# Optimization experiments

Measured on AMD Instinct MI355X. Metric: run time of the kernel, lower is better.

Reference implementation:

```python
import jax, jax.numpy as jnp
import numpy as np


def _segsum(v, idx, n):
    return jax.ops.segment_sum(v, idx, num_segments=n)


def _rdl(z, n_dst, Wna, We, Wi, es, ed, is_, id_):
    """Relationship_Decoupled_layer: node softmax attn + per-edge attn.
    e-channel (mode etype): softmax over 2 logits; i-channel: sigmoid(1 logit)."""
    zd = z[:n_dst]
    node_alpha = jax.nn.softmax(zd @ Wna, axis=1)                      # [nd,2]
    e_e = jax.nn.softmax(jnp.concatenate([z[es], zd[ed]], axis=-1) @ We, axis=1)  # [Ee,2]
    e_i = jax.nn.sigmoid(jnp.concatenate([z[is_], zd[id_]], axis=-1) @ Wi)        # [Ei,1]
    return node_alpha, e_e, e_i


def _one_agg(z, n_dst, W, b, na, e_e, es, ed):
    """One_Neighbor_Aggregation: mean over nbrs of e[:,0]*Linear(z_src), relu, + alpha0*z_dst.
    Linear is applied on src nodes once (linearity) instead of per-edge."""
    zd = na[:, 0:1] * z[:n_dst]
    wz = z @ W + b                                                     # [n_src,D]
    s = _segsum(e_e[:, 0:1] * wz[es], ed, n_dst)                       # [nd,D]
    deg = _segsum(jnp.ones((es.shape[0], 1), z.dtype), ed, n_dst)
    f = jax.nn.relu(s / jnp.maximum(deg, 1.0))
    return f + zd


def _nia(z, n_dst, na, e_e, es, ed, e_i, is_, id_):
    """Neighbor_Interaction_Aggregation: e_h (mode etype, attn col 1) and i_h
    (other etype, sigmoid attn), cross term via polarization identity, + alpha1*z_dst."""
    zd = na[:, 1:2] * z[:n_dst]
    e_h = _segsum(e_e[:, 1:2] * z[es], ed, n_dst)
    i_h = _segsum(e_i * z[is_], id_, n_dst)
    inter = jax.nn.relu(0.5 * (jnp.square(e_h + i_h) - jnp.square(e_h) - jnp.square(i_h)))
    return inter + zd


def setup_inputs() -> dict:
    key = jax.random.key(0)
    ks = jax.random.split(key, 32)
    F, D, O = 256, 128, 64
    n_src0, n_dst0, E0 = 100000, 25000, 500000
    n_src1, n_dst1, E1 = 25000, 5000, 100000

    def ri(k, n, hi):
        return jax.random.randint(k, (n,), 0, hi, dtype=jnp.int32)

    inp = {
        'feat': jax.random.normal(ks[0], (n_src0, F), jnp.float32),
        'src0_cor': ri(ks[1], E0, n_src0), 'dst0_cor': ri(ks[2], E0, n_dst0),
        'src0_sim': ri(ks[3], E0, n_src0), 'dst0_sim': ri(ks[4], E0, n_dst0),
        'src1_cor': ri(ks[5], E1, n_src1), 'dst1_cor': ri(ks[6], E1, n_dst1),
        'src1_sim': ri(ks[7], E1, n_src1), 'dst1_sim': ri(ks[8], E1, n_dst1),
        'n_dst0': n_dst0, 'n_dst1': n_dst1,
    }
    s = 0.05  # keep attention logits / activations in a sane range
    inp['Win'] = jax.random.normal(ks[9], (2, F, D)) * s
    inp['b_in'] = jnp.zeros((2, D), jnp.float32)
    inp['na1'] = jax.random.normal(ks[10], (2, D, 2)) * s
    inp['ea1'] = jax.random.normal(ks[11], (2, 2 * D, 2)) * s
    inp['ia1'] = jax.random.normal(ks[12], (2, 2 * D, 1)) * s
    inp['W1'] = jax.random.normal(ks[13], (2, D, D)) * s
    inp['b1'] = jnp.zeros((2, D), jnp.float32)
    inp['na2'] = jax.random.normal(ks[14], (2, D, 2)) * s
    inp['ea2'] = jax.random.normal(ks[15], (2, 2 * D, 2)) * s
    inp['ia2'] = jax.random.normal(ks[16], (2, 2 * D, 1)) * s
    inp['W2'] = jax.random.normal(ks[17], (2, D, D)) * s
    inp['b2'] = jnp.zeros((2, D), jnp.float32)
    inp['Wout'] = jax.random.normal(ks[18], (2, D, O)) * s
    inp['bout'] = jnp.zeros((2, O), jnp.float32)
    return inp


def reference(feat, src0_cor, dst0_cor, src0_sim, dst0_sim,
              src1_cor, dst1_cor, src1_sim, dst1_sim, n_dst0, n_dst1,
              Win, b_in, na1, ea1, ia1, W1, b1, na2, ea2, ia2, W2, b2, Wout, bout):
    # mode index 0 = 'cor', 1 = 'sim'; e-channel = mode etype, i-channel = other etype
    blk0 = {0: (src0_cor, dst0_cor, src0_sim, dst0_sim),
            1: (src0_sim, dst0_sim, src0_cor, dst0_cor)}
    blk1 = {0: (src1_cor, dst1_cor, src1_sim, dst1_sim),
            1: (src1_sim, dst1_sim, src1_cor, dst1_cor)}
    outs = []
    for m in range(2):
        es0, ed0, is0, id0 = blk0[m]
        es1, ed1, is1, id1 = blk1[m]
        z = feat @ Win[m] + b_in[m]                                    # fc_input (eval: dropout = identity)
        # layer 1 on block0
        na, ee, ei = _rdl(z, n_dst0, na1[m], ea1[m], ia1[m], es0, ed0, is0, id0)
        one = _one_agg(z, n_dst0, W1[m], b1[m], na, ee, es0, ed0)
        nia = _nia(z, n_dst0, na, ee, es0, ed0, ei, is0, id0)
        z = 0.5 * (one + nia)                                          # [n_dst0, D]
        # layer 2 on block1
        na, ee, ei = _rdl(z, n_dst1, na2[m], ea2[m], ia2[m], es1, ed1, is1, id1)
        one = _one_agg(z, n_dst1, W2[m], b2[m], na, ee, es1, ed1)
        nia = _nia(z, n_dst1, na, ee, es1, ed1, ei, is1, id1)
        z = 0.5 * (one + nia)                                          # [n_dst1, D]
        outs.append(z @ Wout[m] + bout[m])
    return jnp.stack(outs)                                             # [2, n_dst1, O] (cor, sim)
```

## Files before the change

### kernel.cpp

```cpp
#include <hip/hip_runtime.h>
#include <hip/hip_bf16.h>
#include <math.h>

#define F_DIM 256
#define D_DIM 128
#define O_DIM 64
#define NS0   100000
#define ND0   25000
#define E0_N  500000
#define NS1   25000
#define ND1   5000
#define E1_N  100000

#define NBE0  1954
#define NBE1  391

typedef __attribute__((ext_vector_type(8))) short s8v;
typedef __attribute__((ext_vector_type(4))) float f4v;

struct CPtr4 { const int *p0, *p1, *p2, *p3; };
struct MPtr4 { int *p0, *p1, *p2, *p3; };

__device__ __forceinline__ float2 unpack2(uint u) {
    union { uint i; float f; } a, b;
    a.i = (u & 0xffffu) << 16; b.i = u & 0xffff0000u;
    return make_float2(a.f, b.f);
}
__device__ __forceinline__ ushort f2bf(float f) {
    __hip_bfloat16 h = __float2bfloat16(f);
    return *(ushort*)&h;
}

__global__ void cvt_bf16(const float* __restrict__ in, ushort* __restrict__ out, int n)
{
    int i = (blockIdx.x * 256 + threadIdx.x) * 4;
    if (i >= n) return;
    float4 v = *(const float4*)(in + i);
    ushort4 o;
    o.x = f2bf(v.x); o.y = f2bf(v.y); o.z = f2bf(v.z); o.w = f2bf(v.w);
    *(ushort4*)(out + i) = o;
}

__global__ void prep_weights(
    const float* __restrict__ Win, const float* __restrict__ W1,
    const float* __restrict__ W2,  const float* __restrict__ Wout,
    ushort* __restrict__ Wtin, ushort* __restrict__ Wt1,
    ushort* __restrict__ Wt2,  ushort* __restrict__ Wtout)
{
    int i = blockIdx.x * 256 + threadIdx.x;
    if (i < 65536) {
        int m = i >> 15, r = i & 32767, k = r >> 7, n = r & 127;
        Wtin[m * 32768 + n * 256 + k] = f2bf(Win[m * 32768 + k * 128 + n]);
    } else if (i < 98304) {
        int i2 = i - 65536;
        int m = i2 >> 14, r = i2 & 16383, k = r >> 7, n = r & 127;
        Wt1[m * 16384 + n * 128 + k] = f2bf(W1[m * 16384 + k * 128 + n]);
    } else if (i < 131072) {
        int i2 = i - 98304;
        int m = i2 >> 14, r = i2 & 16383, k = r >> 7, n = r & 127;
        Wt2[m * 16384 + n * 128 + k] = f2bf(W2[m * 16384 + k * 128 + n]);
    } else if (i < 147456) {
        int i2 = i - 131072;
        int m = i2 >> 13, r = i2 & 8191, k = r >> 6, n = r & 63;
        Wtout[m * 8192 + n * 128 + k] = f2bf(Wout[m * 8192 + k * 64 + n]);
    }
}

template<int NW, int KD, int EPI>
__global__ __launch_bounds__(256) void mfma_gemm(
    const ushort* __restrict__ Ab, size_t astr,
    const ushort* __restrict__ Btb, size_t btstr,
    const float* __restrict__ biasb, size_t bstr,
    const float* __restrict__ cvecb, size_t cvstr,
    const float* __restrict__ partialb, size_t pstr,
    void* __restrict__ Coutb, size_t coutstr, int M)
{
    const int m = blockIdx.y;
    const ushort* A  = Ab + m * astr;
    const ushort* Bt = Btb + m * btstr;
    const float* bias = biasb + m * bstr;
    const float* cvec = (EPI == 2) ? cvecb + m * cvstr : nullptr;
    const float* partial = (EPI == 2) ? partialb + m * pstr : nullptr;
    char* Cout = (char*)Coutb + m * coutstr * (EPI == 1 ? 4 : 2);

    constexpr int PA = 40;
    constexpr int WAVES_M = (NW == 128) ? 2 : 4;
    constexpr int WM = 128 / WAVES_M;
    constexpr int TM = WM / 16;
    constexpr int TN = 4;
    __shared__ ushort As[128 * PA];
    __shared__ ushort Bs[NW * PA];

    const int tid  = threadIdx.x;
    const int row0 = blockIdx.x * 128;
    const int wave = tid >> 6, lane = tid & 63;
    const int l15 = lane & 15, l4 = lane >> 4;
    int wm0, wn0;
    if (NW == 128) { wm0 = (wave >> 1) * 64; wn0 = (wave & 1) * 64; }
    else           { wm0 = wave * WM;        wn0 = 0; }

    f4v acc[TM][TN];
    #pragma unroll
    for (int i = 0; i < TM; ++i)
        #pragma unroll
        for (int j = 0; j < TN; ++j)
            acc[i][j] = (f4v)(0.0f);

    for (int kc = 0; kc < KD; kc += 32) {
        __syncthreads();
        #pragma unroll
        for (int it = 0; it < 2; ++it) {
            int f = tid + it * 256;
            int r = f >> 2, g = (f & 3) * 8;
            int gr = row0 + r;
            float4 v = make_float4(0.f, 0.f, 0.f, 0.f);
            if (gr < M) v = *(const float4*)(A + (size_t)gr * KD + kc + g);
            *(float4*)(&As[r * PA + g]) = v;
        }
        #pragma unroll
        for (int it = 0; it < NW * 32 / (256 * 8); ++it) {
            int f = tid + it * 256;
            int r = f >> 2, g = (f & 3) * 8;
            *(float4*)(&Bs[r * PA + g]) = *(const float4*)(Bt + (size_t)r * KD + kc + g);
        }
        __syncthreads();

        s8v af[TM], bfr[TN];
        #pragma unroll
        for (int i = 0; i < TM; ++i)
            af[i] = *(const s8v*)(&As[(wm0 + i * 16 + l15) * PA + l4 * 8]);
        #pragma unroll
        for (int j = 0; j < TN; ++j)
            bfr[j] = *(const s8v*)(&Bs[(wn0 + j * 16 + l15) * PA + l4 * 8]);
        #pragma unroll
        for (int i = 0; i < TM; ++i)
            #pragma unroll
            for (int j = 0; j < TN; ++j)
                acc[i][j] = __builtin_amdgcn_mfma_f32_16x16x32_bf16(
                    af[i], bfr[j], acc[i][j], 0, 0, 0);
    }

    #pragma unroll
    for (int i = 0; i < TM; ++i) {
        #pragma unroll
        for (int ii = 0; ii < 4; ++ii) {
            int row = row0 + wm0 + i * 16 + l4 * 4 + ii;
            if (row < M) {
                #pragma unroll
                for (int j = 0; j < TN; ++j) {
                    int col = wn0 + j * 16 + l15;
                    float a = acc[i][j][ii];
                    if (EPI == 0) {
                        ((ushort*)Cout)[(size_t)row * NW + col] = f2bf(a + bias[col]);
                    } else if (EPI == 1) {
                        ((float*)Cout)[(size_t)row * NW + col] = a + bias[col];
                    } else {
                        float val = a + cvec[row] * bias[col];
                        float o = partial[(size_t)row * NW + col] + 0.5f * fmaxf(val, 0.f);
                        ((ushort*)Cout)[(size_t)row * NW + col] = f2bf(o);
                    }
                }
            }
        }
    }
}

__global__ void histo4(CPtr4 ed, MPtr4 cnt)
{
    int b = blockIdx.x, t = threadIdx.x;
    const int* edp; int* cp; int e, E;
    if (b < NBE0)          { edp = ed.p0; cp = cnt.p0; e = b * 256 + t;              E = E0_N; }
    else if (b < 2 * NBE0) { edp = ed.p1; cp = cnt.p1; e = (b - NBE0) * 256 + t;     E = E0_N; }
    else if (b < 2 * NBE0 + NBE1)
                           { edp = ed.p2; cp = cnt.p2; e = (b - 2 * NBE0) * 256 + t; E = E1_N; }
    else                   { edp = ed.p3; cp = cnt.p3; e = (b - 2 * NBE0 - NBE1) * 256 + t; E = E1_N; }
    if (e < E) atomicAdd(&cp[edp[e]], 1);
}

__global__ __launch_bounds__(1024) void exscan4(MPtr4 cnt, MPtr4 row, MPtr4 head)
{
    __shared__ int part[1024];
    const int b = blockIdx.x, t = threadIdx.x;
    int* cp; int* rp; int* hp; int n;
    if (b == 0)      { cp = cnt.p0; rp = row.p0; hp = head.p0; n = ND0; }
    else if (b == 1) { cp = cnt.p1; rp = row.p1; hp = head.p1; n = ND0; }
    else if (b == 2) { cp = cnt.p2; rp = row.p2; hp = head.p2; n = ND1; }
    else             { cp = cnt.p3; rp = row.p3; hp = head.p3; n = ND1; }

    const int chunk = (n + 1023) >> 10;
    const int start = t * chunk;
    int s = 0;
    for (int i = 0; i < chunk; ++i) {
        int idx = start + i;
        if (idx < n) s += cp[idx];
    }
    part[t] = s;
    __syncthreads();
    for (int off = 1; off < 1024; off <<= 1) {
        int v = (t >= off) ? part[t - off] : 0;
        __syncthreads();
        part[t] += v;
        __syncthreads();
    }
    int run = (t == 0) ? 0 : part[t - 1];
    for (int i = 0; i < chunk; ++i) {
        int idx = start + i;
        if (idx < n) { rp[idx] = run; hp[idx] = run; run += cp[idx]; }
    }
    if (t == 1023) rp[n] = part[1023];
}

__global__ void build4(CPtr4 es, CPtr4 ed, MPtr4 head, MPtr4 src)
{
    int b = blockIdx.x, t = threadIdx.x;
    const int *esp, *edp; int *hp, *sp; int e, E;
    if (b < NBE0)          { esp = es.p0; edp = ed.p0; hp = head.p0; sp = src.p0; e = b * 256 + t;              E = E0_N; }
    else if (b < 2 * NBE0) { esp = es.p1; edp = ed.p1; hp = head.p1; sp = src.p1; e = (b - NBE0) * 256 + t;     E = E0_N; }
    else if (b < 2 * NBE0 + NBE1)
                           { esp = es.p2; edp = ed.p2; hp = head.p2; sp = src.p2; e = (b - 2 * NBE0) * 256 + t; E = E1_N; }
    else                   { esp = es.p3; edp = ed.p3; hp = head.p3; sp = src.p3; e = (b - 2 * NBE0 - NBE1) * 256 + t; E = E1_N; }
    if (e >= E) return;
    int p = atomicAdd(&hp[edp[e]], 1);
    sp[p] = esp[e];
}

#define NP_NPB 128
__global__ __launch_bounds__(256) void node_proj(
    const ushort* __restrict__ zb, size_t zstr,
    const float* __restrict__ Web,
    const float* __restrict__ Wib,
    float* __restrict__ psb, float* __restrict__ qsb,
    float* __restrict__ pdb, float* __restrict__ qdb,
    int n_src, int n_dst)
{
    const int m = blockIdx.y;
    const ushort* z = zb + m * zstr;
    const float* We = Web + m * 512;
    const float* Wi = Wib + m * 256;
    float* ps = psb + (size_t)m * NS0 * 2;
    float* qs = qsb + (size_t)m * NS0;
    float* pd = pdb + (size_t)m * ND0 * 2;
    float* qd = qdb + (size_t)m * ND0;

    __shared__ float w[6][D_DIM];
    for (int k = threadIdx.x; k < D_DIM; k += 256) {
        w[0][k] = We[k * 2 + 0];
        w[1][k] = We[k * 2 + 1];
        w[2][k] = Wi[k];
        w[3][k] = We[(D_DIM + k) * 2 + 0];
        w[4][k] = We[(D_DIM + k) * 2 + 1];
        w[5][k] = Wi[D_DIM + k];
    }
    __syncthreads();

    const int sub = threadIdx.x & 7;
    const int g   = threadIdx.x >> 3;

    float wr[6][16];
    #pragma unroll
    for (int c = 0; c < 6; ++c)
        #pragma unroll
        for (int q = 0; q < 4; ++q) {
            float4 f = *(const float4*)(&w[c][sub * 16 + q * 4]);
            wr[c][q * 4 + 0] = f.x; wr[c][q * 4 + 1] = f.y;
            wr[c][q * 4 + 2] = f.z; wr[c][q * 4 + 3] = f.w;
        }

    #pragma unroll
    for (int it = 0; it < 4; ++it) {
        int node = blockIdx.x * NP_NPB + it * 32 + g;
        if (node >= n_src) continue;
        const ushort* zp = z + (size_t)node * D_DIM + sub * 16;
        uint4 ra = *(const uint4*)zp;
        uint4 rb = *(const uint4*)(zp + 8);
        uint rr[8] = {ra.x, ra.y, ra.z, ra.w, rb.x, rb.y, rb.z, rb.w};
        float p[6] = {0.f, 0.f, 0.f, 0.f, 0.f, 0.f};
        #pragma unroll
        for (int e = 0; e < 8; ++e) {
            float2 f2 = unpack2(rr[e]);
            #pragma unroll
            for (int c = 0; c < 6; ++c)
                p[c] += f2.x * wr[c][2 * e] + f2.y * wr[c][2 * e + 1];
        }
        #pragma unroll
        for (int off = 4; off > 0; off >>= 1)
            #pragma unroll
            for (int c = 0; c < 6; ++c)
                p[c] += __shfl_down(p[c], off);

        if (sub == 0) {
            *(float2*)(ps + (size_t)node * 2) = make_float2(p[0], p[1]);
            qs[node] = p[2];
            if (node < n_dst) {
                *(float2*)(pd + (size_t)node * 2) = make_float2(p[3], p[4]);
                qd[node] = p[5];
            }
        }
    }
}

__global__ __launch_bounds__(256) void edge_att(
    const float* __restrict__ psb, const float* __restrict__ pdb,
    const float* __restrict__ qsb, const float* __restrict__ qdb,
    const int* __restrict__ row_c, const int* __restrict__ src_c,
    const int* __restrict__ row_s, const int* __restrict__ src_s,
    float* __restrict__ eeb, float* __restrict__ eib, int n_dst)
{
    const int m = blockIdx.y;
    const int d = blockIdx.x * 4 + (threadIdx.x >> 6);
    const int lane = threadIdx.x & 63;
    if (d >= n_dst) return;

    const float* ps = psb + (size_t)m * NS0 * 2;
    const float* qs = qsb + (size_t)m * NS0;
    const float* pdv = pdb + (size_t)m * ND0 * 2;
    const float* qdv = qdb + (size_t)m * ND0;
    const int* erow = m ? row_s : row_c;
    const int* esrc = m ? src_s : src_c;
    const int* irow = m ? row_c : row_s;
    const int* isrc = m ? src_c : src_s;
    float* ee = eeb + (size_t)m * E0_N * 2;
    float* ei = eib + (size_t)m * E0_N;

    const float pd0 = pdv[2 * d], pd1 = pdv[2 * d + 1];
    const float qdd = qdv[d];

    const int b0 = erow[d], b1 = erow[d + 1];
    for (int j = b0 + lane; j < b1; j += 64) {
        int s = esrc[j];
        float2 pp = *(const float2*)(ps + 2 * (size_t)s);
        float l0 = pp.x + pd0, l1 = pp.y + pd1;
        float mx = fmaxf(l0, l1);
        float x0 = __expf(l0 - mx), x1 = __expf(l1 - mx);
        float inv = 1.0f / (x0 + x1);
        *(float2*)(ee + 2 * (size_t)j) = make_float2(x0 * inv, x1 * inv);
    }
    const int c0 = irow[d], c1 = irow[d + 1];
    for (int j = c0 + lane; j < c1; j += 64) {
        float q = qs[isrc[j]] + qdd;
        ei[j] = 1.0f / (1.0f + __expf(-q));
    }
}

__global__ __launch_bounds__(256) void gather_acc(
    const ushort* __restrict__ zb, size_t zstr,
    const float* __restrict__ eeb, const float* __restrict__ eib,
    const int* __restrict__ row_c, const int* __restrict__ src_c,
    const int* __restrict__ row_s, const int* __restrict__ src_s,
    ushort* __restrict__ h0base, float* __restrict__ cvecb,
    float* __restrict__ partialb, int n_dst)
{
    const int m = blockIdx.y;
    const int d = blockIdx.x * 4 + (threadIdx.x >> 6);
    const int lane = threadIdx.x & 63;
    if (d >= n_dst) return;

    const ushort* z = zb + m * zstr;
    const float* ee = eeb + (size_t)m * E0_N * 2;
    const float* ei = eib + (size_t)m * E0_N;
    const int* erow = m ? row_s : row_c;
    const int* esrc = m ? src_s : src_c;
    const int* irow = m ? row_c : row_s;
    const int* isrc = m ? src_c : src_s;
    ushort* h0b = h0base + (size_t)m * ND0 * D_DIM;
    float* cvec = cvecb + (size_t)m * ND0;
    float* partial = partialb + (size_t)m * ND0 * D_DIM;

    float h0x = 0.f, h0y = 0.f, ehx = 0.f, ehy = 0.f;
    float ihx = 0.f, ihy = 0.f, se0 = 0.f;

    const int b0 = erow[d], b1 = erow[d + 1];
    int j = b0;
    for (; j + 8 <= b1; j += 8) {
        int sdx[8]; float2 ww[8]; uint rr[8];
        #pragma unroll
        for (int k = 0; k < 8; ++k) sdx[k] = esrc[j + k];
        #pragma unroll
        for (int k = 0; k < 8; ++k) ww[k] = *(const float2*)(ee + 2 * (size_t)(j + k));
        #pragma unroll
        for (int k = 0; k < 8; ++k) rr[k] = *(const uint*)(z + (size_t)sdx[k] * D_DIM + lane * 2);
        #pragma unroll
        for (int k = 0; k < 8; ++k) {
            float2 v = unpack2(rr[k]);
            h0x += ww[k].x * v.x; h0y += ww[k].x * v.y;
            ehx += ww[k].y * v.x; ehy += ww[k].y * v.y;
            se0 += ww[k].x;
        }
    }
    for (; j < b1; ++j) {
        int s = esrc[j];
        float2 w = *(const float2*)(ee + 2 * (size_t)j);
        float2 v = unpack2(*(const uint*)(z + (size_t)s * D_DIM + lane * 2));
        h0x += w.x * v.x; h0y += w.x * v.y;
        ehx += w.y * v.x; ehy += w.y * v.y;
        se0 += w.x;
    }

    const int c0 = irow[d], c1 = irow[d + 1];
    j = c0;
    for (; j + 8 <= c1; j += 8) {
        int sdx[8]; float gg[8]; uint rr[8];
        #pragma unroll
        for (int k = 0; k < 8; ++k) sdx[k] = isrc[j + k];
        #pragma unroll
        for (int k = 0; k < 8; ++k) gg[k] = ei[j + k];
        #pragma unroll
        for (int k = 0; k < 8; ++k) rr[k] = *(const uint*)(z + (size_t)sdx[k] * D_DIM + lane * 2);
        #pragma unroll
        for (int k = 0; k < 8; ++k) {
            float2 v = unpack2(rr[k]);
            ihx += gg[k] * v.x; ihy += gg[k] * v.y;
        }
    }
    for (; j < c1; ++j) {
        int s = isrc[j];
        float g = ei[j];
        float2 v = unpack2(*(const uint*)(z + (size_t)s * D_DIM + lane * 2));
        ihx += g * v.x; ihy += g * v.y;
    }

    float inv = 1.0f / fmaxf((float)(b1 - b0), 1.0f);
    uint hp = (uint)f2bf(h0x * inv) | ((uint)f2bf(h0y * inv) << 16);
    *(uint*)(h0b + (size_t)d * D_DIM + lane * 2) = hp;
    if (lane == 0) cvec[d] = se0 * inv;

    float2 zd = unpack2(*(const uint*)(z + (size_t)d * D_DIM + lane * 2));
    float px = 0.5f * (fmaxf(ehx * ihx, 0.f) + zd.x);
    float py = 0.5f * (fmaxf(ehy * ihy, 0.f) + zd.y);
    *(float2*)(partial + (size_t)d * D_DIM + lane * 2) = make_float2(px, py);
}

extern "C" void kernel_launch(void* const* d_in, const int* in_sizes, int n_in,
                              void* d_out, int out_size, void* d_ws, size_t ws_size,
                              hipStream_t stream)
{
    const float* feat = (const float*)d_in[0];
    const int* src0_cor = (const int*)d_in[1];
    const int* dst0_cor = (const int*)d_in[2];
    const int* src0_sim = (const int*)d_in[3];
    const int* dst0_sim = (const int*)d_in[4];
    const int* src1_cor = (const int*)d_in[5];
    const int* dst1_cor = (const int*)d_in[6];
    const int* src1_sim = (const int*)d_in[7];
    const int* dst1_sim = (const int*)d_in[8];
    const float* Win  = (const float*)d_in[11];
    const float* b_in = (const float*)d_in[12];
    const float* ea1  = (const float*)d_in[14];
    const float* ia1  = (const float*)d_in[15];
    const float* W1   = (const float*)d_in[16];
    const float* b1   = (const float*)d_in[17];
    const float* ea2  = (const float*)d_in[19];
    const float* ia2  = (const float*)d_in[20];
    const float* W2   = (const float*)d_in[21];
    const float* b2   = (const float*)d_in[22];
    const float* Wout = (const float*)d_in[23];
    const float* bout = (const float*)d_in[24];
    (void)in_sizes; (void)n_in; (void)out_size; (void)ws_size;

    char* wsb = (char*)d_ws;
    size_t off = 0;
    auto alloc_f = [&](size_t n) { float*  p = (float*) (wsb + off); off += n * 4; return p; };
    auto alloc_i = [&](size_t n) { int*    p = (int*)   (wsb + off); off += n * 4; return p; };
    auto alloc_h = [&](size_t n) { ushort* p = (ushort*)(wsb + off); off += ((n * 2 + 15) & ~15ull); return p; };

    ushort* featb = alloc_h((size_t)NS0 * F_DIM);
    ushort* z0b   = alloc_h((size_t)2 * NS0 * D_DIM);
    ushort* z1b   = alloc_h((size_t)2 * NS1 * D_DIM);
    ushort* z2b   = alloc_h((size_t)2 * ND1 * D_DIM);
    ushort* h0b   = alloc_h((size_t)2 * ND0 * D_DIM);
    ushort* Wtin  = alloc_h((size_t)2 * D_DIM * F_DIM);
    ushort* Wt1   = alloc_h((size_t)2 * D_DIM * D_DIM);
    ushort* Wt2   = alloc_h((size_t)2 * D_DIM * D_DIM);
    ushort* Wtout = alloc_h((size_t)2 * O_DIM * D_DIM);

    float* ps      = alloc_f((size_t)2 * NS0 * 2);
    float* qs      = alloc_f((size_t)2 * NS0);
    float* pd      = alloc_f((size_t)2 * ND0 * 2);
    float* qd      = alloc_f((size_t)2 * ND0);
    float* cvec    = alloc_f((size_t)2 * ND0);
    float* partial = alloc_f((size_t)2 * ND0 * D_DIM);
    float* ee      = alloc_f((size_t)2 * E0_N * 2);
    float* ei      = alloc_f((size_t)2 * E0_N);

    int* src_c0 = alloc_i(E0_N); int* row_c0 = alloc_i(ND0 + 1);
    int* src_s0 = alloc_i(E0_N); int* row_s0 = alloc_i(ND0 + 1);
    int* src_c1 = alloc_i(E1_N); int* row_c1 = alloc_i(ND1 + 1);
    int* src_s1 = alloc_i(E1_N); int* row_s1 = alloc_i(ND1 + 1);
    int* cnt_all  = alloc_i(2 * ND0 + 2 * ND1);
    int* head_all = alloc_i(2 * ND0 + 2 * ND1);

    int* cnt_c0 = cnt_all;            int* head_c0 = head_all;
    int* cnt_s0 = cnt_all + ND0;      int* head_s0 = head_all + ND0;
    int* cnt_c1 = cnt_all + 2 * ND0;  int* head_c1 = head_all + 2 * ND0;
    int* cnt_s1 = cnt_c1 + ND1;       int* head_s1 = head_c1 + ND1;

    const int NB_ALL = 2 * NBE0 + 2 * NBE1;
    hipMemsetAsync(cnt_all, 0, (size_t)(2 * ND0 + 2 * ND1) * 4, stream);
    {
        CPtr4 edp  = {dst0_cor, dst0_sim, dst1_cor, dst1_sim};
        CPtr4 esp  = {src0_cor, src0_sim, src1_cor, src1_sim};
        MPtr4 cntp = {cnt_c0, cnt_s0, cnt_c1, cnt_s1};
        MPtr4 rowp = {row_c0, row_s0, row_c1, row_s1};
        MPtr4 hdp  = {head_c0, head_s0, head_c1, head_s1};
        MPtr4 srcp = {src_c0, src_s0, src_c1, src_s1};
        histo4<<<NB_ALL, 256, 0, stream>>>(edp, cntp);
        exscan4<<<4, 1024, 0, stream>>>(cntp, rowp, hdp);
        build4<<<NB_ALL, 256, 0, stream>>>(esp, edp, hdp, srcp);
    }

    cvt_bf16<<<((size_t)NS0 * F_DIM / 4 + 255) / 256, 256, 0, stream>>>(
        feat, featb, NS0 * F_DIM);
    prep_weights<<<576, 256, 0, stream>>>(Win, W1, W2, Wout, Wtin, Wt1, Wt2, Wtout);

    const size_t Z0S = (size_t)NS0 * D_DIM, Z1S = (size_t)NS1 * D_DIM;
    const size_t Z2S = (size_t)ND1 * D_DIM, H0S = (size_t)ND0 * D_DIM;

    mfma_gemm<128, 256, 0><<<dim3((NS0 + 127) / 128, 2), 256, 0, stream>>>(
        featb, 0, Wtin, (size_t)D_DIM * F_DIM, b_in, D_DIM,
        nullptr, 0, nullptr, 0, z0b, Z0S, NS0);

    node_proj<<<dim3((NS0 + NP_NPB - 1) / NP_NPB, 2), 256, 0, stream>>>(
        z0b, Z0S, ea1, ia1, ps, qs, pd, qd, NS0, ND0);
    edge_att<<<dim3((ND0 + 3) / 4, 2), 256, 0, stream>>>(
        ps, pd, qs, qd, row_c0, src_c0, row_s0, src_s0, ee, ei, ND0);
    gather_acc<<<dim3((ND0 + 3) / 4, 2), 256, 0, stream>>>(
        z0b, Z0S, ee, ei, row_c0, src_c0, row_s0, src_s0,
        h0b, cvec, partial, ND0);
    mfma_gemm<128, 128, 2><<<dim3((ND0 + 127) / 128, 2), 256, 0, stream>>>(
        h0b, H0S, Wt1, (size_t)D_DIM * D_DIM, b1, D_DIM,
        cvec, ND0, partial, H0S, z1b, Z1S, ND0);

    node_proj<<<dim3((NS1 + NP_NPB - 1) / NP_NPB, 2), 256, 0, stream>>>(
        z1b, Z1S, ea2, ia2, ps, qs, pd, qd, NS1, ND1);
    edge_att<<<dim3((ND1 + 3) / 4, 2), 256, 0, stream>>>(
        ps, pd, qs, qd, row_c1, src_c1, row_s1, src_s1, ee, ei, ND1);
    gather_acc<<<dim3((ND1 + 3) / 4, 2), 256, 0, stream>>>(
        z1b, Z1S, ee, ei, row_c1, src_c1, row_s1, src_s1,
        h0b, cvec, partial, ND1);
    mfma_gemm<128, 128, 2><<<dim3((ND1 + 127) / 128, 2), 256, 0, stream>>>(
        h0b, H0S, Wt2, (size_t)D_DIM * D_DIM, b2, D_DIM,
        cvec, ND0, partial, H0S, z2b, Z2S, ND1);

    mfma_gemm<64, 128, 1><<<dim3((ND1 + 127) / 128, 2), 256, 0, stream>>>(
        z2b, Z2S, Wtout, (size_t)O_DIM * D_DIM, bout, O_DIM,
        nullptr, 0, nullptr, 0, (float*)d_out, (size_t)ND1 * O_DIM, ND1);
}
```

Measured before the change: 595.7 us.

## Fuse fp32-to-bf16 conversion into input GEMM and pack edge weights with indices

Removes the separate feat-to-bf16 conversion kernel and converts fp32 A tiles to bf16 while loading them inside the input GEMM. edge_att now writes packed (weight, src index) pairs and computes the per-destination mean of e0, so gather_acc reads one 8-byte record per edge instead of separate index and weight arrays. gather_acc derives e_h as the plain sum minus the e0-weighted sum, using the fact that the two softmax weights add to one. The input GEMM now reads twice as many A bytes per tile, and the subtraction trick may change rounding slightly.

```diff
diff --git a/kernel.cpp b/kernel.cpp
--- a/kernel.cpp
+++ b/kernel.cpp
@@ -30,15 +30,11 @@
     __hip_bfloat16 h = __float2bfloat16(f);
     return *(ushort*)&h;
 }
-
-__global__ void cvt_bf16(const float* __restrict__ in, ushort* __restrict__ out, int n)
-{
-    int i = (blockIdx.x * 256 + threadIdx.x) * 4;
-    if (i >= n) return;
-    float4 v = *(const float4*)(in + i);
-    ushort4 o;
-    o.x = f2bf(v.x); o.y = f2bf(v.y); o.z = f2bf(v.z); o.w = f2bf(v.w);
-    *(ushort4*)(out + i) = o;
+__device__ __forceinline__ float u2f(uint u) {
+    union { uint i; float f; } v; v.i = u; return v.f;
+}
+__device__ __forceinline__ uint f2u(float f) {
+    union { uint i; float f; } v; v.f = f; return v.i;
 }
 
 __global__ void prep_weights(
@@ -66,9 +62,9 @@
     }
 }
 
-template<int NW, int KD, int EPI>
+template<int NW, int KD, int EPI, bool AF32>
 __global__ __launch_bounds__(256) void mfma_gemm(
-    const ushort* __restrict__ Ab, size_t astr,
+    const void* __restrict__ Ab, size_t astr,
     const ushort* __restrict__ Btb, size_t btstr,
     const float* __restrict__ biasb, size_t bstr,
     const float* __restrict__ cvecb, size_t cvstr,
@@ -76,7 +72,8 @@
     void* __restrict__ Coutb, size_t coutstr, int M)
 {
     const int m = blockIdx.y;
-    const ushort* A  = Ab + m * astr;
+    const ushort* A16 = AF32 ? nullptr : ((const ushort*)Ab + m * astr);
+    const float*  A32 = AF32 ? ((const float*)Ab + m * astr) : nullptr;
     const ushort* Bt = Btb + m * btstr;
     const float* bias = biasb + m * bstr;
     const float* cvec = (EPI == 2) ? cvecb + m * cvstr : nullptr;
@@ -113,9 +110,23 @@
             int f = tid + it * 256;
             int r = f >> 2, g = (f & 3) * 8;
             int gr = row0 + r;
-            float4 v = make_float4(0.f, 0.f, 0.f, 0.f);
-            if (gr < M) v = *(const float4*)(A + (size_t)gr * KD + kc + g);
-            *(float4*)(&As[r * PA + g]) = v;
+            if (AF32) {
+                float4 v0 = make_float4(0.f, 0.f, 0.f, 0.f);
+                float4 v1 = make_float4(0.f, 0.f, 0.f, 0.f);
+                if (gr < M) {
+                    v0 = *(const float4*)(A32 + (size_t)gr * KD + kc + g);
+                    v1 = *(const float4*)(A32 + (size_t)gr * KD + kc + g + 4);
+                }
+                ushort4 o0, o1;
+                o0.x = f2bf(v0.x); o0.y = f2bf(v0.y); o0.z = f2bf(v0.z); o0.w = f2bf(v0.w);
+                o1.x = f2bf(v1.x); o1.y = f2bf(v1.y); o1.z = f2bf(v1.z); o1.w = f2bf(v1.w);
+                *(ushort4*)(&As[r * PA + g]) = o0;
+                *(ushort4*)(&As[r * PA + g + 4]) = o1;
+            } else {
+                float4 v = make_float4(0.f, 0.f, 0.f, 0.f);
+                if (gr < M) v = *(const float4*)(A16 + (size_t)gr * KD + kc + g);
+                *(float4*)(&As[r * PA + g]) = v;
+            }
         }
         #pragma unroll
         for (int it = 0; it < NW * 32 / (256 * 8); ++it) {
@@ -304,7 +315,8 @@
     const float* __restrict__ qsb, const float* __restrict__ qdb,
     const int* __restrict__ row_c, const int* __restrict__ src_c,
     const int* __restrict__ row_s, const int* __restrict__ src_s,
-    float* __restrict__ eeb, float* __restrict__ eib, int n_dst)
+    uint2* __restrict__ epkb, uint2* __restrict__ ipkb,
+    float* __restrict__ cvecb, int n_dst)
 {
     const int m = blockIdx.y;
     const int d = blockIdx.x * 4 + (threadIdx.x >> 6);
@@ -319,36 +331,44 @@
     const int* esrc = m ? src_s : src_c;
     const int* irow = m ? row_c : row_s;
     const int* isrc = m ? src_c : src_s;
-    float* ee = eeb + (size_t)m * E0_N * 2;
-    float* ei = eib + (size_t)m * E0_N;
+    uint2* epk = epkb + (size_t)m * E0_N;
+    uint2* ipk = ipkb + (size_t)m * E0_N;
+    float* cvec = cvecb + (size_t)m * ND0;
 
     const float pd0 = pdv[2 * d], pd1 = pdv[2 * d + 1];
     const float qdd = qdv[d];
 
     const int b0 = erow[d], b1 = erow[d + 1];
+    float se0 = 0.f;
     for (int j = b0 + lane; j < b1; j += 64) {
         int s = esrc[j];
         float2 pp = *(const float2*)(ps + 2 * (size_t)s);
         float l0 = pp.x + pd0, l1 = pp.y + pd1;
         float mx = fmaxf(l0, l1);
         float x0 = __expf(l0 - mx), x1 = __expf(l1 - mx);
-        float inv = 1.0f / (x0 + x1);
-        *(float2*)(ee + 2 * (size_t)j) = make_float2(x0 * inv, x1 * inv);
-    }
+        float e0 = x0 / (x0 + x1);
+        epk[j] = make_uint2(f2u(e0), (uint)s);
+        se0 += e0;
+    }
+    #pragma unroll
+    for (int off = 32; off > 0; off >>= 1)
+        se0 += __shfl_down(se0, off);
+    if (lane == 0) cvec[d] = se0 / fmaxf((float)(b1 - b0), 1.0f);
+
     const int c0 = irow[d], c1 = irow[d + 1];
     for (int j = c0 + lane; j < c1; j += 64) {
-        float q = qs[isrc[j]] + qdd;
-        ei[j] = 1.0f / (1.0f + __expf(-q));
+        int s = isrc[j];
+        float q = qs[s] + qdd;
+        float sg = 1.0f / (1.0f + __expf(-q));
+        ipk[j] = make_uint2(f2u(sg), (uint)s);
     }
 }
 
 __global__ __launch_bounds__(256) void gather_acc(
     const ushort* __restrict__ zb, size_t zstr,
-    const float* __restrict__ eeb, const float* __restrict__ eib,
-    const int* __restrict__ row_c, const int* __restrict__ src_c,
-    const int* __restrict__ row_s, const int* __restrict__ src_s,
-    ushort* __restrict__ h0base, float* __restrict__ cvecb,
-    float* __restrict__ partialb, int n_dst)
+    const uint2* __restrict__ epkb, const uint2* __restrict__ ipkb,
+    const int* __restrict__ row_c, const int* __restrict__ row_s,
+    ushort* __restrict__ h0base, float* __restrict__ partialb, int n_dst)
 {
     const int m = blockIdx.y;
     const int d = blockIdx.x * 4 + (threadIdx.x >> 6);
@@ -356,73 +376,66 @@
     if (d >= n_dst) return;
 
     const ushort* z = zb + m * zstr;
-    const float* ee = eeb + (size_t)m * E0_N * 2;
-    const float* ei = eib + (size_t)m * E0_N;
+    const uint2* epk = epkb + (size_t)m * E0_N;
+    const uint2* ipk = ipkb + (size_t)m * E0_N;
     const int* erow = m ? row_s : row_c;
-    const int* esrc = m ? src_s : src_c;
     const int* irow = m ? row_c : row_s;
-    const int* isrc = m ? src_c : src_s;
     ushort* h0b = h0base + (size_t)m * ND0 * D_DIM;
-    float* cvec = cvecb + (size_t)m * ND0;
     float* partial = partialb + (size_t)m * ND0 * D_DIM;
 
-    float h0x = 0.f, h0y = 0.f, ehx = 0.f, ehy = 0.f;
-    float ihx = 0.f, ihy = 0.f, se0 = 0.f;
+    float h0x = 0.f, h0y = 0.f, szx = 0.f, szy = 0.f;
+    float ihx = 0.f, ihy = 0.f;
 
     const int b0 = erow[d], b1 = erow[d + 1];
     int j = b0;
     for (; j + 8 <= b1; j += 8) {
-        int sdx[8]; float2 ww[8]; uint rr[8];
-        #pragma unroll
-        for (int k = 0; k < 8; ++k) sdx[k] = esrc[j + k];
-        #pragma unroll
-        for (int k = 0; k < 8; ++k) ww[k] = *(const float2*)(ee + 2 * (size_t)(j + k));
-        #pragma unroll
-        for (int k = 0; k < 8; ++k) rr[k] = *(const uint*)(z + (size_t)sdx[k] * D_DIM + lane * 2);
+        uint2 ew[8]; uint rr[8];
+        #pragma unroll
+        for (int k = 0; k < 8; ++k) ew[k] = epk[j + k];
+        #pragma unroll
+        for (int k = 0; k < 8; ++k) rr[k] = *(const uint*)(z + (size_t)ew[k].y * D_DIM + lane * 2);
         #pragma unroll
         for (int k = 0; k < 8; ++k) {
+            float w0 = u2f(ew[k].x);
             float2 v = unpack2(rr[k]);
-            h0x += ww[k].x * v.x; h0y += ww[k].x * v.y;
-            ehx += ww[k].y * v.x; ehy += ww[k].y * v.y;
-            se0 += ww[k].x;
+            szx += v.x; szy += v.y;
+            h0x += w0 * v.x; h0y += w0 * v.y;
         }
     }
     for (; j < b1; ++j) {
-        int s = esrc[j];
-        float2 w = *(const float2*)(ee + 2 * (size_t)j);
-        float2 v = unpack2(*(const uint*)(z + (size_t)s * D_DIM + lane * 2));
-        h0x += w.x * v.x; h0y += w.x * v.y;
-        ehx += w.y * v.x; ehy += w.y * v.y;
-        se0 += w.x;
+        uint2 ew = epk[j];
+        float w0 = u2f(ew.x);
+        float2 v = unpack2(*(const uint*)(z + (size_t)ew.y * D_DIM + lane * 2));
+        szx += v.x; szy += v.y;
+        h0x += w0 * v.x; h0y += w0 * v.y;
     }
 
     const int c0 = irow[d], c1 = irow[d + 1];
     j = c0;
     for (; j + 8 <= c1; j += 8) {
-        int sdx[8]; float gg[8]; uint rr[8];
-        #pragma unroll
-        for (int k = 0; k < 8; ++k) sdx[k] = isrc[j + k];
-        #pragma unroll
-        for (int k = 0; k < 8; ++k) gg[k] = ei[j + k];
-        #pragma unroll
-        for (int k = 0; k < 8; ++k) rr[k] = *(const uint*)(z + (size_t)sdx[k] * D_DIM + lane * 2);
+        uint2 ew[8]; uint rr[8];
+        #pragma unroll
+        for (int k = 0; k < 8; ++k) ew[k] = ipk[j + k];
+        #pragma unroll
+        for (int k = 0; k < 8; ++k) rr[k] = *(const uint*)(z + (size_t)ew[k].y * D_DIM + lane * 2);
         #pragma unroll
         for (int k = 0; k < 8; ++k) {
+            float g = u2f(ew[k].x);
             float2 v = unpack2(rr[k]);
-            ihx += gg[k] * v.x; ihy += gg[k] * v.y;
+            ihx += g * v.x; ihy += g * v.y;
         }
     }
     for (; j < c1; ++j) {
-        int s = isrc[j];
-        float g = ei[j];
-        float2 v = unpack2(*(const uint*)(z + (size_t)s * D_DIM + lane * 2));
+        uint2 ew = ipk[j];
+        float g = u2f(ew.x);
+        float2 v = unpack2(*(const uint*)(z + (size_t)ew.y * D_DIM + lane * 2));
         ihx += g * v.x; ihy += g * v.y;
     }
 
+    float ehx = szx - h0x, ehy = szy - h0y;
     float inv = 1.0f / fmaxf((float)(b1 - b0), 1.0f);
     uint hp = (uint)f2bf(h0x * inv) | ((uint)f2bf(h0y * inv) << 16);
     *(uint*)(h0b + (size_t)d * D_DIM + lane * 2) = hp;
-    if (lane == 0) cvec[d] = se0 * inv;
 
     float2 zd = unpack2(*(const uint*)(z + (size_t)d * D_DIM + lane * 2));
     float px = 0.5f * (fmaxf(ehx * ihx, 0.f) + zd.x);
@@ -462,8 +475,8 @@
     auto alloc_f = [&](size_t n) { float*  p = (float*) (wsb + off); off += n * 4; return p; };
     auto alloc_i = [&](size_t n) { int*    p = (int*)   (wsb + off); off += n * 4; return p; };
     auto alloc_h = [&](size_t n) { ushort* p = (ushort*)(wsb + off); off += ((n * 2 + 15) & ~15ull); return p; };
-
-    ushort* featb = alloc_h((size_t)NS0 * F_DIM);
+    auto alloc_u2 = [&](size_t n) { uint2* p = (uint2*)(wsb + off); off += n * 8; return p; };
+
     ushort* z0b   = alloc_h((size_t)2 * NS0 * D_DIM);
     ushort* z1b   = alloc_h((size_t)2 * NS1 * D_DIM);
     ushort* z2b   = alloc_h((size_t)2 * ND1 * D_DIM);
@@ -479,8 +492,8 @@
     float* qd      = alloc_f((size_t)2 * ND0);
     float* cvec    = alloc_f((size_t)2 * ND0);
     float* partial = alloc_f((size_t)2 * ND0 * D_DIM);
-    float* ee      = alloc_f((size_t)2 * E0_N * 2);
-    float* ei      = alloc_f((size_t)2 * E0_N);
+    uint2* epk     = alloc_u2((size_t)2 * E0_N);
+    uint2* ipk     = alloc_u2((size_t)2 * E0_N);
 
     int* src_c0 = alloc_i(E0_N); int* row_c0 = alloc_i(ND0 + 1);
     int* src_s0 = alloc_i(E0_N); int* row_s0 = alloc_i(ND0 + 1);
@@ -508,40 +521,36 @@
         build4<<<NB_ALL, 256, 0, stream>>>(esp, edp, hdp, srcp);
     }
 
-    cvt_bf16<<<((size_t)NS0 * F_DIM / 4 + 255) / 256, 256, 0, stream>>>(
-        feat, featb, NS0 * F_DIM);
     prep_weights<<<576, 256, 0, stream>>>(Win, W1, W2, Wout, Wtin, Wt1, Wt2, Wtout);
 
     const size_t Z0S = (size_t)NS0 * D_DIM, Z1S = (size_t)NS1 * D_DIM;
     const size_t Z2S = (size_t)ND1 * D_DIM, H0S = (size_t)ND0 * D_DIM;
 
-    mfma_gemm<128, 256, 0><<<dim3((NS0 + 127) / 128, 2), 256, 0, stream>>>(
-        featb, 0, Wtin, (size_t)D_DIM * F_DIM, b_in, D_DIM,
+    mfma_gemm<128, 256, 0, true><<<dim3((NS0 + 127) / 128, 2), 256, 0, stream>>>(
+        feat, 0, Wtin, (size_t)D_DIM * F_DIM, b_in, D_DIM,
         nullptr, 0, nullptr, 0, z0b, Z0S, NS0);
 
     node_proj<<<dim3((NS0 + NP_NPB - 1) / NP_NPB, 2), 256, 0, stream>>>(
         z0b, Z0S, ea1, ia1, ps, qs, pd, qd, NS0, ND0);
     edge_att<<<dim3((ND0 + 3) / 4, 2), 256, 0, stream>>>(
-        ps, pd, qs, qd, row_c0, src_c0, row_s0, src_s0, ee, ei, ND0);
+        ps, pd, qs, qd, row_c0, src_c0, row_s0, src_s0, epk, ipk, cvec, ND0);
     gather_acc<<<dim3((ND0 + 3) / 4, 2), 256, 0, stream>>>(
-        z0b, Z0S, ee, ei, row_c0, src_c0, row_s0, src_s0,
-        h0b, cvec, partial, ND0);
-    mfma_gemm<128, 128, 2><<<dim3((ND0 + 127) / 128, 2), 256, 0, stream>>>(
+        z0b, Z0S, epk, ipk, row_c0, row_s0, h0b, partial, ND0);
+    mfma_gemm<128, 128, 2, false><<<dim3((ND0 + 127) / 128, 2), 256, 0, stream>>>(
         h0b, H0S, Wt1, (size_t)D_DIM * D_DIM, b1, D_DIM,
         cvec, ND0, partial, H0S, z1b, Z1S, ND0);
 
     node_proj<<<dim3((NS1 + NP_NPB - 1) / NP_NPB, 2), 256, 0, stream>>>(
         z1b, Z1S, ea2, ia2, ps, qs, pd, qd, NS1, ND1);
     edge_att<<<dim3((ND1 + 3) / 4, 2), 256, 0, stream>>>(
-        ps, pd, qs, qd, row_c1, src_c1, row_s1, src_s1, ee, ei, ND1);
+        ps, pd, qs, qd, row_c1, src_c1, row_s1, src_s1, epk, ipk, cvec, ND1);
     gather_acc<<<dim3((ND1 + 3) / 4, 2), 256, 0, stream>>>(
-        z1b, Z1S, ee, ei, row_c1, src_c1, row_s1, src_s1,
-        h0b, cvec, partial, ND1);
-    mfma_gemm<128, 128, 2><<<dim3((ND1 + 127) / 128, 2), 256, 0, stream>>>(
+        z1b, Z1S, epk, ipk, row_c1, row_s1, h0b, partial, ND1);
+    mfma_gemm<128, 128, 2, false><<<dim3((ND1 + 127) / 128, 2), 256, 0, stream>>>(
         h0b, H0S, Wt2, (size_t)D_DIM * D_DIM, b2, D_DIM,
         cvec, ND0, partial, H0S, z2b, Z2S, ND1);
 
-    mfma_gemm<64, 128, 1><<<dim3((ND1 + 127) / 128, 2), 256, 0, stream>>>(
+    mfma_gemm<64, 128, 1, false><<<dim3((ND1 + 127) / 128, 2), 256, 0, stream>>>(
         z2b, Z2S, Wtout, (size_t)O_DIM * D_DIM, bout, O_DIM,
         nullptr, 0, nullptr, 0, (float*)d_out, (size_t)ND1 * O_DIM, ND1);
 }
```

Result: no change. 588.5 us (-1.2%).
